# Performance work log

Measured on AMD Instinct MI355X. Metric: run time of the kernel, lower is better.

## Reference

```python
import jax, jax.numpy as jnp
import numpy as np

TEMP = 0.07  # temperature used as logits / 0.07 in the original


def setup_inputs() -> dict:
    key = jax.random.key(0)
    k1, k2, k3 = jax.random.split(key, 3)
    B, N, T, L, D = 8, 128, 8, 6, 256
    meta = jax.random.normal(k1, (B, N, T, L, D), dtype=jnp.float32)
    thing = jax.random.randint(k2, (B, N, T), 0, 2, dtype=jnp.int32)
    label = jax.random.randint(k3, (B, N, T), 0, 40, dtype=jnp.int32)
    return {"meta_weight_for_con": meta, "thing_gt_idx": thing, "label_tmp": label}


def _con_loss(meta, thing, label):
    # meta: [B,N,T,L,D]; thing,label: [B,N,T]
    B, N, T, L, D = meta.shape
    P = N * T
    valid = thing.reshape(B, P).astype(bool)            # [B,P] boolean gt mask
    lab = label.reshape(B, P)                           # [B,P]
    # meta_weight_b[mask] -> [K,L,D]; permute(1,0,2) -> per-layer [K,D].
    # We keep all P positions and mask instead of compacting (jit-friendly).
    w = meta.reshape(B, P, L, D).transpose(0, 2, 1, 3)  # [B,L,P,D]
    w = w / jnp.maximum(jnp.linalg.norm(w, axis=-1, keepdims=True), 1e-12)  # F.normalize
    z = jnp.einsum('blpd,blqd->blpq', w, w) / TEMP      # similarity / temp [B,L,P,P]

    same = lab[:, :, None] == lab[:, None, :]           # [B,P,P]
    vpair = valid[:, :, None] & valid[:, None, :]
    eye = jnp.eye(P, dtype=bool)
    pos_mask = same & (~eye) & vpair                    # positives: same label, not self
    neg_mask = (~same) & vpair                          # negatives: different label

    K = valid.sum(axis=1)                               # [B] ins_num_ per batch
    pos_count = pos_mask.sum(axis=-1)                   # [B,P]
    neg_count = neg_mask.sum(axis=-1)                   # [B,P]

    # --- random positive sample per (batch, layer, row), mirroring np.random.choice ---
    u = jax.random.uniform(jax.random.key(42), (B, L, P))
    r = jnp.floor(u * pos_count[:, None, :].astype(u.dtype)).astype(jnp.int32)
    r = jnp.minimum(r, jnp.maximum(pos_count - 1, 0)[:, None, :])
    ranks = jnp.cumsum(pos_mask, axis=-1) - 1           # rank of each positive in index order
    sel = pos_mask[:, None, :, :] & (ranks[:, None, :, :] == r[..., None])  # [B,L,P,P]
    zp = jnp.sum(jnp.where(sel, z, 0.0), axis=-1)       # chosen positive logit [B,L,P]
    diag = jnp.diagonal(z, axis1=-2, axis2=-1)          # self-sim fallback when no positives
    zp = jnp.where((pos_count > 0)[:, None, :], zp, diag)

    # --- last negative (original pads by repeating the last negative to K-1) ---
    iota = jnp.arange(P)
    idx_last = jnp.max(jnp.where(neg_mask, iota[None, None, :], -1), axis=-1)  # [B,P]
    idx = jnp.broadcast_to(jnp.maximum(idx_last, 0)[:, None, :, None], (B, L, P, 1))
    zl = jnp.take_along_axis(z, idx, axis=-1)[..., 0]   # [B,L,P]

    # --- stable CE with label 0: loss = lse(logits) - zp ---
    max_n = jnp.max(jnp.where(neg_mask[:, None], z, -jnp.inf), axis=-1)  # [B,L,P]
    m = jnp.maximum(zp, max_n)
    m = jnp.where(jnp.isfinite(m), m, zp)
    sum_neg = jnp.sum(jnp.where(neg_mask[:, None], jnp.exp(z - m[..., None]), 0.0), axis=-1)
    pad = jnp.maximum((K[:, None] - 1 - neg_count), 0).astype(z.dtype)   # [B,P]
    pad_term = pad[:, None, :] * jnp.where((neg_count > 0)[:, None, :], jnp.exp(zl - m), 0.0)
    loss_row = m + jnp.log(jnp.exp(zp - m) + sum_neg + pad_term) - zp    # [B,L,P]

    row_w = valid.astype(z.dtype)
    mean_per = jnp.sum(loss_row * row_w[:, None, :], axis=-1) / jnp.maximum(K, 1)[:, None].astype(z.dtype)  # [B,L]

    gate = jnp.sum((thing.sum(axis=2) > 0), axis=1) >= 2  # skip batches with <2 gt rows
    return jnp.sum(jnp.where(gate[:, None], mean_per, 0.0))


def reference(meta_weight_for_con, thing_gt_idx, label_tmp):
    return _con_loss(meta_weight_for_con, thing_gt_idx, label_tmp)
```

## Files before the change

kernel.cpp:

```cpp
#include <hip/hip_runtime.h>
#include <stdint.h>

namespace {

constexpr int Bb = 8, Ll = 6, Dd = 256, Pp = 1024;
constexpr float SCALE_Y = 14.285714285714286f * 1.4426950408889634f;
constexpr float M0y = 21.0f;
constexpr float LN2f = 0.6931471805599453f;

typedef __attribute__((ext_vector_type(8))) short short8;
typedef __attribute__((ext_vector_type(4))) float floatx4;

__device__ __forceinline__ void async16(const void* g, void* l) {
  __builtin_amdgcn_global_load_lds(
      (const __attribute__((address_space(1))) void*)g,
      (__attribute__((address_space(3))) void*)l, 16, 0, 0);
}

__device__ __forceinline__ uint32_t rotl32(uint32_t x, int n) {
  return (x << n) | (x >> (32 - n));
}
__device__ __forceinline__ void tf_round(uint32_t& x0, uint32_t& x1, int r) {
  x0 += x1; x1 = rotl32(x1, r); x1 ^= x0;
}
__device__ void threefry2x32(uint32_t x0, uint32_t x1, uint32_t& o0, uint32_t& o1) {
  const uint32_t k0 = 0u, k1 = 42u;
  const uint32_t k2 = k0 ^ k1 ^ 0x1BD11BDAu;
  x0 += k0; x1 += k1;
  tf_round(x0,x1,13); tf_round(x0,x1,15); tf_round(x0,x1,26); tf_round(x0,x1,6);
  x0 += k1; x1 += k2 + 1u;
  tf_round(x0,x1,17); tf_round(x0,x1,29); tf_round(x0,x1,16); tf_round(x0,x1,24);
  x0 += k2; x1 += k0 + 2u;
  tf_round(x0,x1,13); tf_round(x0,x1,15); tf_round(x0,x1,26); tf_round(x0,x1,6);
  x0 += k0; x1 += k1 + 3u;
  tf_round(x0,x1,17); tf_round(x0,x1,29); tf_round(x0,x1,16); tf_round(x0,x1,24);
  x0 += k1; x1 += k2 + 4u;
  tf_round(x0,x1,13); tf_round(x0,x1,15); tf_round(x0,x1,26); tf_round(x0,x1,6);
  x0 += k2; x1 += k0 + 5u;
  o0 = x0; o1 = x1;
}
__device__ float jax_u01(uint32_t idx) {
  const uint32_t HALF = (uint32_t)(Bb * Ll * Pp / 2);
  uint32_t o0, o1, bits;
  if (idx < HALF) { threefry2x32(idx, idx + HALF, o0, o1); bits = o0; }
  else            { threefry2x32(idx - HALF, idx, o0, o1); bits = o1; }
  return __uint_as_float((bits >> 9) | 0x3f800000u) - 1.0f;
}

__device__ __forceinline__ unsigned short bf16rne(float x) {
  uint32_t u = __float_as_uint(x);
  return (unsigned short)((u + 0x7FFFu + ((u >> 16) & 1u)) >> 16);
}
__device__ __forceinline__ float bf16tof(unsigned short h) {
  return __uint_as_float(((uint32_t)h) << 16);
}

constexpr int NB_NORM = Bb * Pp * Ll / 4;
constexpr int NB_ROW  = Bb * Pp / 4;

__global__ void prep_k(const float* __restrict__ meta, const int* __restrict__ thing,
                       const int* __restrict__ label, unsigned short* __restrict__ wn,
                       int* __restrict__ qpos, int* __restrict__ negc,
                       int* __restrict__ qidx, int* __restrict__ Kv,
                       int* __restrict__ gatev, float* __restrict__ rowsum_g,
                       float* __restrict__ out) {
  __shared__ int sK[256], sG[256];
  const int bid = blockIdx.x, t = threadIdx.x;

  if (bid < NB_NORM) {
    const int wid = (bid * 256 + t) >> 6;
    const int lane = t & 63;
    const float4 v = *(const float4*)(meta + (size_t)wid * Dd + lane * 4);
    float ss = v.x * v.x + v.y * v.y + v.z * v.z + v.w * v.w;
    #pragma unroll
    for (int m = 32; m; m >>= 1) ss += __shfl_xor(ss, m, 64);
    const float inv = 1.0f / fmaxf(sqrtf(ss), 1e-12f);
    const int bp = wid / Ll, l = wid - bp * Ll;
    const int b = bp >> 10, p = bp & (Pp - 1);
    unsigned short* dst = wn + ((size_t)(b * Ll + l) * Pp + p) * Dd + lane * 4;
    ushort4 o;
    o.x = bf16rne(v.x * inv); o.y = bf16rne(v.y * inv);
    o.z = bf16rne(v.z * inv); o.w = bf16rne(v.w * inv);
    *(ushort4*)dst = o;
    return;
  }
  if (bid < NB_NORM + NB_ROW) {
    const int wid = (bid - NB_NORM) * 4 + (t >> 6);
    const int lane = t & 63;
    const int b = wid >> 10, p = wid & (Pp - 1);
    const int* lab = label + b * Pp;
    const int* th  = thing + b * Pp;
    const int myLab = lab[p];
    const bool myValid = (th[p] != 0);

    uint32_t posbits = 0;
    int cnt[16];
    int pc = 0, nc = 0, last = -1;
    #pragma unroll
    for (int c = 0; c < 16; ++c) {
      const int q = c * 64 + lane;
      const int lq = lab[q];
      const bool vq = (th[q] != 0);
      const bool same = (lq == myLab);
      const bool pos = myValid && vq && same && (q != p);
      const bool neg = myValid && vq && !same;
      uint64_t bp2 = __ballot(pos);
      uint64_t bn = __ballot(neg);
      if (pos) posbits |= (1u << c);
      cnt[c] = __popcll(bp2);
      pc += cnt[c];
      nc += __popcll(bn);
      if (bn) last = c * 64 + 63 - __clzll(bn);
    }
    int qsel[Ll];
    #pragma unroll
    for (int l = 0; l < Ll; ++l) qsel[l] = p;
    if (pc > 0) {
      for (int l = 0; l < Ll; ++l) {
        const float u = jax_u01((uint32_t)((b * Ll + l) * Pp + p));
        int r = (int)floorf(u * (float)pc);
        r = min(r, pc - 1);
        int base = 0;
        for (int c = 0; c < 16; ++c) {
          if (r < base + cnt[c]) {
            const bool mine = (posbits >> c) & 1u;
            uint64_t bm = __ballot(mine);
            uint64_t ltmask = (lane == 0) ? 0ull : (~0ull >> (64 - lane));
            int myrank = __popcll(bm & ltmask);
            bool hit = mine && (base + myrank == r);
            uint64_t hb = __ballot(hit);
            qsel[l] = c * 64 + (int)__builtin_ctzll(hb);
            break;
          }
          base += cnt[c];
        }
      }
    }
    if (lane == 0) {
      negc[wid] = nc;
      qidx[wid] = (last < 0) ? 0 : last;
      #pragma unroll
      for (int l = 0; l < Ll; ++l) qpos[(b * Ll + l) * Pp + p] = qsel[l];
    }
    return;
  }
  if (bid < NB_NORM + NB_ROW + Bb) {
    const int b = bid - (NB_NORM + NB_ROW);
    int k = 0;
    for (int p = t; p < Pp; p += 256) k += (thing[b * Pp + p] != 0);
    int g = 0;
    if (t < 128) {
      int any = 0;
      for (int tt = 0; tt < 8; ++tt) any |= (thing[(b * 128 + t) * 8 + tt] != 0);
      g = any;
    }
    sK[t] = k; sG[t] = g;
    __syncthreads();
    for (int s = 128; s; s >>= 1) {
      if (t < s) { sK[t] += sK[t + s]; sG[t] += sG[t + s]; }
      __syncthreads();
    }
    if (t == 0) { Kv[b] = sK[0]; gatev[b] = (sG[0] >= 2) ? 1 : 0; }
    return;
  }
  if (bid < NB_NORM + NB_ROW + Bb + 48) {
    const int idx = (bid - (NB_NORM + NB_ROW + Bb)) * 256 + t;
    *(float4*)(rowsum_g + idx * 4) = (float4){0.f, 0.f, 0.f, 0.f};
    return;
  }
  if (t == 0) out[0] = 0.f;
}

__global__ void zpzl_k(const unsigned short* __restrict__ wn,
                       const int* __restrict__ qpos, const int* __restrict__ qidx,
                       float* __restrict__ zp_g, float* __restrict__ zl_g) {
  const int wid = blockIdx.x * 4 + (threadIdx.x >> 6);
  const int lane = threadIdx.x & 63;
  const int bl = wid >> 10, p = wid & (Pp - 1);
  const int b = bl / Ll;
  const int qp = qpos[bl * Pp + p];
  const int qi = qidx[b * Pp + p];
  const unsigned short* W = wn + (size_t)bl * Pp * Dd;
  const ushort4 a  = *(const ushort4*)(W + (size_t)p  * Dd + lane * 4);
  const ushort4 vb = *(const ushort4*)(W + (size_t)qp * Dd + lane * 4);
  const ushort4 vc = *(const ushort4*)(W + (size_t)qi * Dd + lane * 4);
  const float ax = bf16tof(a.x), ay = bf16tof(a.y), az = bf16tof(a.z), aw = bf16tof(a.w);
  float sp = ax * bf16tof(vb.x) + ay * bf16tof(vb.y) + az * bf16tof(vb.z) + aw * bf16tof(vb.w);
  float sl = ax * bf16tof(vc.x) + ay * bf16tof(vc.y) + az * bf16tof(vc.z) + aw * bf16tof(vc.w);
  #pragma unroll
  for (int m = 32; m; m >>= 1) {
    sp += __shfl_xor(sp, m, 64);
    sl += __shfl_xor(sl, m, 64);
  }
  if (lane == 0) {
    zp_g[bl * Pp + p] = sp * SCALE_Y;
    zl_g[bl * Pp + p] = sl * SCALE_Y;
  }
}

__global__ __launch_bounds__(256)
void gemm_loss_k(const unsigned short* __restrict__ wn,
                 const int* __restrict__ thing, const int* __restrict__ label,
                 float* __restrict__ rowsum_g) {
  __shared__ __align__(16) unsigned short As[128 * 64];
  __shared__ __align__(16) unsigned short Bs[128 * 64];
  __shared__ int labp_s[128], clab_s[128], cval_s[128];
  __shared__ float rowsum_lds[128];

  const int t = threadIdx.x;
  const int bl = blockIdx.z;
  const int b = bl / Ll;
  const int p0 = blockIdx.x * 128, q0 = blockIdx.y * 128;

  if (t < 128) {
    labp_s[t] = label[b * Pp + p0 + t];
    clab_s[t] = label[b * Pp + q0 + t];
    cval_s[t] = thing[b * Pp + q0 + t];
    rowsum_lds[t] = 0.f;
  }

  const unsigned short* Wbl = wn + (size_t)bl * Pp * Dd;
  const int lane = t & 63;
  const int w = t >> 6, wr = w >> 1, wc = w & 1;
  const int cq = lane & 15, rq = lane >> 4;
  const int wbase16 = (t & ~63) * 16;

  floatx4 acc[4][4];
  #pragma unroll
  for (int i = 0; i < 4; ++i)
    #pragma unroll
    for (int j = 0; j < 4; ++j) acc[i][j] = (floatx4){0.f, 0.f, 0.f, 0.f};

  for (int k0 = 0; k0 < Dd; k0 += 64) {
    __syncthreads();
    #pragma unroll
    for (int it = 0; it < 4; ++it) {
      const int c = it * 256 + t;
      const int row = c >> 3, sp = c & 7;
      const int sl = sp ^ (row & 7);
      async16(Wbl + (size_t)(p0 + row) * Dd + k0 + sl * 8, (char*)As + it * 4096 + wbase16);
      async16(Wbl + (size_t)(q0 + row) * Dd + k0 + sl * 8, (char*)Bs + it * 4096 + wbase16);
    }
    __syncthreads();
    #pragma unroll
    for (int sub = 0; sub < 2; ++sub) {
      short8 af[4], bf[4];
      #pragma unroll
      for (int fi = 0; fi < 4; ++fi) {
        const int row = wr * 64 + fi * 16 + cq;
        const int sp = (sub * 4 + rq) ^ (row & 7);
        af[fi] = *(const short8*)((const char*)As + row * 128 + sp * 16);
      }
      #pragma unroll
      for (int fj = 0; fj < 4; ++fj) {
        const int row = wc * 64 + fj * 16 + cq;
        const int sp = (sub * 4 + rq) ^ (row & 7);
        bf[fj] = *(const short8*)((const char*)Bs + row * 128 + sp * 16);
      }
      #pragma unroll
      for (int fi = 0; fi < 4; ++fi)
        #pragma unroll
        for (int fj = 0; fj < 4; ++fj)
          acc[fi][fj] = __builtin_amdgcn_mfma_f32_16x16x32_bf16(af[fi], bf[fj],
                                                                acc[fi][fj], 0, 0, 0);
    }
  }

  int qlabv[4];
  float qvalf[4];
  #pragma unroll
  for (int fj = 0; fj < 4; ++fj) {
    const int cl = wc * 64 + fj * 16 + cq;
    qlabv[fj] = clab_s[cl];
    qvalf[fj] = cval_s[cl] ? 1.f : 0.f;
  }
  #pragma unroll
  for (int fi = 0; fi < 4; ++fi) {
    #pragma unroll
    for (int reg = 0; reg < 4; ++reg) {
      const int rl = wr * 64 + fi * 16 + rq * 4 + reg;
      const int rlab = labp_s[rl];
      float rsum = 0.f;
      #pragma unroll
      for (int fj = 0; fj < 4; ++fj) {
        const float y = acc[fi][fj][reg] * SCALE_Y;
        const float negm = (qlabv[fj] != rlab) ? qvalf[fj] : 0.f;
        rsum += negm * exp2f(y - M0y);
      }
      rsum += __shfl_xor(rsum, 1); rsum += __shfl_xor(rsum, 2);
      rsum += __shfl_xor(rsum, 4); rsum += __shfl_xor(rsum, 8);
      if (cq == 0) atomicAdd(&rowsum_lds[rl], rsum);
    }
  }
  __syncthreads();
  if (t < 128) atomicAdd(&rowsum_g[bl * Pp + p0 + t], rowsum_lds[t]);
}

__global__ void finalize_k(const float* __restrict__ rowsum_g, const float* __restrict__ zp_g,
                           const float* __restrict__ zl_g, const int* __restrict__ negc,
                           const int* __restrict__ thing, const int* __restrict__ Kv,
                           const int* __restrict__ gatev, float* __restrict__ out) {
  const int bl = blockIdx.x, b = bl / Ll, t = threadIdx.x;
  const int Kb = Kv[b];
  const float invK = 1.f / (float)max(Kb, 1);
  float acc = 0.f;
  for (int p = t; p < Pp; p += 256) {
    if (thing[b * Pp + p] != 0) {
      const float yp = zp_g[bl * Pp + p], yl = zl_g[bl * Pp + p];
      const float rs = rowsum_g[bl * Pp + p];
      const int nc = negc[b * Pp + p];
      const float pad = fmaxf((float)(Kb - 1 - nc), 0.f);
      const float tot = exp2f(yp - M0y) + rs + ((nc > 0) ? pad * exp2f(yl - M0y) : 0.f);
      acc += LN2f * (M0y + log2f(tot) - yp) * invK;
    }
  }
  __shared__ float sb[256];
  sb[t] = acc;
  __syncthreads();
  for (int s = 128; s; s >>= 1) {
    if (t < s) sb[t] += sb[t + s];
    __syncthreads();
  }
  if (t == 0 && gatev[b]) atomicAdd(out, sb[0]);
}

}

extern "C" void kernel_launch(void* const* d_in, const int* in_sizes, int n_in,
                              void* d_out, int out_size, void* d_ws, size_t ws_size,
                              hipStream_t stream) {
  const float* meta = (const float*)d_in[0];
  const int* thing  = (const int*)d_in[1];
  const int* label  = (const int*)d_in[2];
  float* out = (float*)d_out;

  char* ws = (char*)d_ws;
  size_t off = 0;
  unsigned short* wn = (unsigned short*)(ws + off); off += (size_t)Bb * Ll * Pp * Dd * 2;
  int* qpos  = (int*)(ws + off); off += (size_t)Bb * Ll * Pp * 4;
  int* negc  = (int*)(ws + off); off += (size_t)Bb * Pp * 4;
  int* qidx  = (int*)(ws + off); off += (size_t)Bb * Pp * 4;
  int* Kv    = (int*)(ws + off); off += 64;
  int* gatev = (int*)(ws + off); off += 64;
  float* rowsum_g = (float*)(ws + off); off += (size_t)Bb * Ll * Pp * 4;
  float* zp_g     = (float*)(ws + off); off += (size_t)Bb * Ll * Pp * 4;
  float* zl_g     = (float*)(ws + off); off += (size_t)Bb * Ll * Pp * 4;

  const int nb_prep = NB_NORM + NB_ROW + Bb + 48 + 1;
  prep_k<<<nb_prep, 256, 0, stream>>>(meta, thing, label, wn, qpos, negc, qidx,
                                      Kv, gatev, rowsum_g, out);
  zpzl_k<<<(Bb * Ll * Pp) / 4, 256, 0, stream>>>(wn, qpos, qidx, zp_g, zl_g);
  {
    dim3 grid(Pp / 128, Pp / 128, Bb * Ll);
    gemm_loss_k<<<grid, 256, 0, stream>>>(wn, thing, label, rowsum_g);
  }
  finalize_k<<<Bb * Ll, 256, 0, stream>>>(rowsum_g, zp_g, zl_g, negc, thing, Kv, gatev, out);
}
```

Before: 166.2 us.

## Exploit Gram matrix symmetry: compute upper-triangle tiles and scatter column sums

The similarity matrix W·Wᵀ is symmetric, so the GEMM grid now covers only the 36 upper-triangular 128x128 tile pairs per (batch, layer) instead of all 64. Each off-diagonal tile adds both its row sums and its column sums (with a symmetric mask that now includes the row validity) into the global row-sum buffer. Diagonal tiles load only one operand into LDS and reuse it for both sides. This cuts MFMA work and global loads by nearly half, at the cost of extra column reductions, more atomics, and some load imbalance between diagonal and off-diagonal blocks.

```diff
diff --git a/kernel.cpp b/kernel.cpp
--- a/kernel.cpp
+++ b/kernel.cpp
@@ -10,6 +10,17 @@
 
 typedef __attribute__((ext_vector_type(8))) short short8;
 typedef __attribute__((ext_vector_type(4))) float floatx4;
+
+__device__ const int PAIRS[36] = {
+  0x00,0x01,0x02,0x03,0x04,0x05,0x06,0x07,
+  0x11,0x12,0x13,0x14,0x15,0x16,0x17,
+  0x22,0x23,0x24,0x25,0x26,0x27,
+  0x33,0x34,0x35,0x36,0x37,
+  0x44,0x45,0x46,0x47,
+  0x55,0x56,0x57,
+  0x66,0x67,
+  0x77
+};
 
 __device__ __forceinline__ void async16(const void* g, void* l) {
   __builtin_amdgcn_global_load_lds(
@@ -204,19 +215,24 @@
                  float* __restrict__ rowsum_g) {
   __shared__ __align__(16) unsigned short As[128 * 64];
   __shared__ __align__(16) unsigned short Bs[128 * 64];
-  __shared__ int labp_s[128], clab_s[128], cval_s[128];
-  __shared__ float rowsum_lds[128];
+  __shared__ int labp_s[128], valp_s[128], labq_s[128], valq_s[128];
+  __shared__ float rowsum_lds[128], colsum_lds[128];
 
   const int t = threadIdx.x;
-  const int bl = blockIdx.z;
+  const int bl = blockIdx.y;
   const int b = bl / Ll;
-  const int p0 = blockIdx.x * 128, q0 = blockIdx.y * 128;
+  const int pair = PAIRS[blockIdx.x];
+  const int pt = pair >> 4, qt = pair & 15;
+  const bool diag = (pt == qt);
+  const int p0 = pt * 128, q0 = qt * 128;
 
   if (t < 128) {
     labp_s[t] = label[b * Pp + p0 + t];
-    clab_s[t] = label[b * Pp + q0 + t];
-    cval_s[t] = thing[b * Pp + q0 + t];
+    valp_s[t] = thing[b * Pp + p0 + t];
+    labq_s[t] = label[b * Pp + q0 + t];
+    valq_s[t] = thing[b * Pp + q0 + t];
     rowsum_lds[t] = 0.f;
+    colsum_lds[t] = 0.f;
   }
 
   const unsigned short* Wbl = wn + (size_t)bl * Pp * Dd;
@@ -231,6 +247,8 @@
     #pragma unroll
     for (int j = 0; j < 4; ++j) acc[i][j] = (floatx4){0.f, 0.f, 0.f, 0.f};
 
+  const char* Bbase = diag ? (const char*)As : (const char*)Bs;
+
   for (int k0 = 0; k0 < Dd; k0 += 64) {
     __syncthreads();
     #pragma unroll
@@ -239,7 +257,8 @@
       const int row = c >> 3, sp = c & 7;
       const int sl = sp ^ (row & 7);
       async16(Wbl + (size_t)(p0 + row) * Dd + k0 + sl * 8, (char*)As + it * 4096 + wbase16);
-      async16(Wbl + (size_t)(q0 + row) * Dd + k0 + sl * 8, (char*)Bs + it * 4096 + wbase16);
+      if (!diag)
+        async16(Wbl + (size_t)(q0 + row) * Dd + k0 + sl * 8, (char*)Bs + it * 4096 + wbase16);
     }
     __syncthreads();
     #pragma unroll
@@ -255,7 +274,7 @@
       for (int fj = 0; fj < 4; ++fj) {
         const int row = wc * 64 + fj * 16 + cq;
         const int sp = (sub * 4 + rq) ^ (row & 7);
-        bf[fj] = *(const short8*)((const char*)Bs + row * 128 + sp * 16);
+        bf[fj] = *(const short8*)(Bbase + row * 128 + sp * 16);
       }
       #pragma unroll
       for (int fi = 0; fi < 4; ++fi)
@@ -268,11 +287,12 @@
 
   int qlabv[4];
   float qvalf[4];
+  float csum[4] = {0.f, 0.f, 0.f, 0.f};
   #pragma unroll
   for (int fj = 0; fj < 4; ++fj) {
     const int cl = wc * 64 + fj * 16 + cq;
-    qlabv[fj] = clab_s[cl];
-    qvalf[fj] = cval_s[cl] ? 1.f : 0.f;
+    qlabv[fj] = labq_s[cl];
+    qvalf[fj] = valq_s[cl] ? 1.f : 0.f;
   }
   #pragma unroll
   for (int fi = 0; fi < 4; ++fi) {
@@ -280,20 +300,34 @@
     for (int reg = 0; reg < 4; ++reg) {
       const int rl = wr * 64 + fi * 16 + rq * 4 + reg;
       const int rlab = labp_s[rl];
+      const float rvalf = valp_s[rl] ? 1.f : 0.f;
       float rsum = 0.f;
       #pragma unroll
       for (int fj = 0; fj < 4; ++fj) {
         const float y = acc[fi][fj][reg] * SCALE_Y;
-        const float negm = (qlabv[fj] != rlab) ? qvalf[fj] : 0.f;
-        rsum += negm * exp2f(y - M0y);
+        const float negm = (qlabv[fj] != rlab) ? (qvalf[fj] * rvalf) : 0.f;
+        const float term = negm * exp2f(y - M0y);
+        rsum += term;
+        csum[fj] += term;
       }
       rsum += __shfl_xor(rsum, 1); rsum += __shfl_xor(rsum, 2);
       rsum += __shfl_xor(rsum, 4); rsum += __shfl_xor(rsum, 8);
       if (cq == 0) atomicAdd(&rowsum_lds[rl], rsum);
     }
   }
+  if (!diag) {
+    #pragma unroll
+    for (int fj = 0; fj < 4; ++fj) {
+      float c = csum[fj];
+      c += __shfl_xor(c, 16); c += __shfl_xor(c, 32);
+      if (rq == 0) atomicAdd(&colsum_lds[wc * 64 + fj * 16 + cq], c);
+    }
+  }
   __syncthreads();
-  if (t < 128) atomicAdd(&rowsum_g[bl * Pp + p0 + t], rowsum_lds[t]);
+  if (t < 128) {
+    atomicAdd(&rowsum_g[bl * Pp + p0 + t], rowsum_lds[t]);
+    if (!diag) atomicAdd(&rowsum_g[bl * Pp + q0 + t], colsum_lds[t]);
+  }
 }
 
 __global__ void finalize_k(const float* __restrict__ rowsum_g, const float* __restrict__ zp_g,
@@ -351,7 +385,7 @@
                                       Kv, gatev, rowsum_g, out);
   zpzl_k<<<(Bb * Ll * Pp) / 4, 256, 0, stream>>>(wn, qpos, qidx, zp_g, zl_g);
   {
-    dim3 grid(Pp / 128, Pp / 128, Bb * Ll);
+    dim3 grid(36, Bb * Ll);
     gemm_loss_k<<<grid, 256, 0, stream>>>(wn, thing, label, rowsum_g);
   }
   finalize_k<<<Bb * Ll, 256, 0, stream>>>(rowsum_g, zp_g, zl_g, negc, thing, Kv, gatev, out);
```

Measured after the change: 163.0 us. No clear change (-1.9%).
